# Performance work log

Hardware: AMD Instinct MI355X
Metric: run time of the kernel (lower is better)

The kernel has to match this reference:

```python
import jax, jax.numpy as jnp
import numpy as np

N_AGENT = 32768   # number of agent (dst) nodes
MAX_NBRS = 16     # fixed neighbor count per agent (pad target)
N_NBR = N_AGENT * MAX_NBRS   # nbr (src) nodes
E = N_AGENT * MAX_NBRS       # 1hop edges (grouped by dst)
F_NBR, F_AGENT, F_HOP = 32, 32, 8
H = 128           # critic_hidden_size
N_POW = 4         # n_pow_opts


def _lin(key, fin, fout):
    return jax.random.normal(key, (fin, fout), jnp.float32) / np.sqrt(fin)


def setup_inputs() -> dict:
    key = jax.random.key(0)
    ks = jax.random.split(key, 12)
    return {
        "feat_nbr": jax.random.normal(ks[0], (N_NBR, F_NBR), jnp.float32),
        "feat_agent": jax.random.normal(ks[1], (N_AGENT, F_AGENT), jnp.float32),
        "edge_feat": jax.random.normal(ks[2], (E, F_HOP), jnp.float32),
        "h": jnp.zeros((N_AGENT, H), jnp.float32),
        # NodeGNBlock '1hop': message MLP + update MLP
        "W_msg": _lin(ks[3], F_NBR + F_HOP, H), "b_msg": jnp.zeros((H,), jnp.float32),
        "W_upd": _lin(ks[4], H + F_AGENT, H), "b_upd": jnp.zeros((H,), jnp.float32),
        # RnnLayer: GRUCell(H, H)
        "W_x": _lin(ks[5], H, 3 * H), "W_h": _lin(ks[6], H, 3 * H),
        "b_ih": jnp.zeros((3 * H,), jnp.float32), "b_hh": jnp.zeros((3 * H,), jnp.float32),
        # EdgeGNBlock f_out: edge MLP -> per-edge q over power options, plus agent head
        "W_e1": _lin(ks[7], F_NBR + H + F_HOP, H), "b_e1": jnp.zeros((H,), jnp.float32),
        "W_e2": _lin(ks[8], H, N_POW), "b_e2": jnp.zeros((N_POW,), jnp.float32),
        "W_a": _lin(ks[9], 2 * H, 1), "b_a": jnp.zeros((1,), jnp.float32),
        # graph: each agent has exactly MAX_NBRS incident edges, grouped by dst
        "src_idx": jax.random.randint(ks[10], (E,), 0, N_NBR),
        "dst_idx": jnp.repeat(jnp.arange(N_AGENT), MAX_NBRS),
    }


def reference(feat_nbr, feat_agent, edge_feat, h,
              W_msg, b_msg, W_upd, b_upd,
              W_x, W_h, b_ih, b_hh,
              W_e1, b_e1, W_e2, b_e2, W_a, b_a,
              src_idx, dst_idx):
    act = jax.nn.relu
    # --- NodeGNBlock '1hop': edge message -> sum-aggregate -> node update ---
    m = act(jnp.concatenate([feat_nbr[src_idx], edge_feat], axis=1) @ W_msg + b_msg)  # [E,H]
    agg = jax.ops.segment_sum(m, dst_idx, num_segments=N_AGENT, indices_are_sorted=True)  # [N,H]
    x = act(jnp.concatenate([agg, feat_agent], axis=1) @ W_upd + b_upd)  # [N,H]
    # --- RnnLayer: GRUCell step; output x == new hidden ---
    gi = x @ W_x + b_ih
    gh = h @ W_h + b_hh
    ir, iz, inn = jnp.split(gi, 3, axis=1)
    hr, hz, hn = jnp.split(gh, 3, axis=1)
    r = jax.nn.sigmoid(ir + hr)
    z = jax.nn.sigmoid(iz + hz)
    n = jnp.tanh(inn + r * hn)
    h_new = (1.0 - z) * n + z * h  # [N,H]
    # --- EdgeGNBlock f_out: per-edge q-values + per-agent scalar ---
    ze = act(jnp.concatenate([feat_nbr[src_idx], h_new[dst_idx], edge_feat], axis=1) @ W_e1 + b_e1)  # [E,H]
    nbr_out = ze @ W_e2 + b_e2  # [E, N_POW]
    agg2 = jax.ops.segment_sum(ze, dst_idx, num_segments=N_AGENT, indices_are_sorted=True)
    agent_out = jnp.concatenate([agg2, h_new], axis=1) @ W_a + b_a  # [N,1]
    # --- pad_edge_output: edges grouped by dst with fixed degree -> reshape ---
    padded_nbr_out = nbr_out.reshape(N_AGENT, MAX_NBRS * N_POW)
    q_vals = jnp.concatenate([padded_nbr_out, agent_out], axis=1)  # [N, MAX_NBRS*N_POW+1]
    return q_vals, h_new
```

## Files before the change

### kernel.cpp

```cpp
#include <hip/hip_runtime.h>

typedef _Float16 half_t;
typedef half_t half8 __attribute__((ext_vector_type(8)));
typedef half_t half4 __attribute__((ext_vector_type(4)));
typedef float f32x4 __attribute__((ext_vector_type(4)));
typedef __attribute__((address_space(1))) const void gc_t;
typedef __attribute__((address_space(3))) void ls_t;

#define NAGENT 32768
#define MAXN   16
#define HD     128
#define QCOLS  65
#define QN     (NAGENT * QCOLS)
#define AGB    16
#define EPB    (AGB * MAXN)

#define O_WMT   0
#define O_WE1E  8192
#define O_WE1H  16384
#define O_WUPD  32768
#define O_WX    53248
#define O_WH    102400
#define W_TOTAL 151552

#define MFMA(a, b, c) __builtin_amdgcn_mfma_f32_16x16x32_f16((a), (b), (c), 0, 0, 0)

__global__ void prep_weights(const float* __restrict__ W_msg, const float* __restrict__ W_upd,
                             const float* __restrict__ W_x, const float* __restrict__ W_h,
                             const float* __restrict__ W_e1, half_t* __restrict__ ws) {
    int i = blockIdx.x * 256 + threadIdx.x;
    if (i >= W_TOTAL) return;
    float v; int dst;
    if (i < 8192) {
        int k = i >> 7, n = i & 127;
        v = (k < 40) ? W_msg[k * HD + n] : 0.f;
        dst = O_WMT + n * 64 + k;
    } else if (i < 16384) {
        int j = i - 8192; int k = j >> 7, n = j & 127;
        v = (k < 32) ? W_e1[k * HD + n] : (k < 40 ? W_e1[(160 + k - 32) * HD + n] : 0.f);
        dst = O_WE1E + n * 64 + k;
    } else if (i < 32768) {
        int j = i - 16384; int k = j >> 7, n = j & 127;
        v = W_e1[(32 + k) * HD + n];
        dst = O_WE1H + n * 128 + k;
    } else if (i < 53248) {
        int j = i - 32768; int k = j >> 7, n = j & 127;
        v = W_upd[k * HD + n];
        dst = O_WUPD + n * 160 + k;
    } else if (i < 102400) {
        int j = i - 53248; int k = j / 384, n = j - k * 384;
        v = W_x[k * 384 + n];
        dst = O_WX + n * 128 + k;
    } else {
        int j = i - 102400; int k = j / 384, n = j - k * 384;
        v = W_h[k * 384 + n];
        dst = O_WH + n * 128 + k;
    }
    ws[dst] = (half_t)v;
}

__device__ __forceinline__ half8 ldB(const half_t* __restrict__ WT, int kstride, int n0, int k0, int l) {
    return *(const half8*)(WT + (size_t)(n0 + (l & 15)) * kstride + k0 + ((l >> 4) * 8));
}
__device__ __forceinline__ half4 cvt4(float4 v) {
    return (half4){(half_t)v.x, (half_t)v.y, (half_t)v.z, (half_t)v.w};
}
__device__ __forceinline__ half8 cvt8(float4 a, float4 b) {
    return (half8){(half_t)a.x, (half_t)a.y, (half_t)a.z, (half_t)a.w,
                   (half_t)b.x, (half_t)b.y, (half_t)b.z, (half_t)b.w};
}
__device__ __forceinline__ float sigm(float x) { return 1.f / (1.f + __expf(-x)); }
__device__ __forceinline__ float tanh_fast(float x) { return 1.f - 2.f / (__expf(2.f * x) + 1.f); }

__global__ __launch_bounds__(256, 3) void k_fused(
    const float* __restrict__ feat_nbr, const float* __restrict__ feat_agent,
    const float* __restrict__ edge_feat, const float* __restrict__ h_in,
    const float* __restrict__ b_msg, const float* __restrict__ b_upd,
    const float* __restrict__ b_ih, const float* __restrict__ b_hh,
    const float* __restrict__ b_e1, const float* __restrict__ W_e2,
    const float* __restrict__ b_e2, const float* __restrict__ W_a,
    const float* __restrict__ b_a, const int* __restrict__ src_idx,
    const half_t* __restrict__ ws, float* __restrict__ out)
{
    const int t = threadIdx.x;
    const int w = t >> 6, l = t & 63;
    const int l16 = l & 15, q = l >> 4;
    const int a0 = blockIdx.x * AGB;
    const int be = blockIdx.x * EPB;
    const half8 hz = {0, 0, 0, 0, 0, 0, 0, 0};

    __shared__ float  fng[4][8][64][4];
    __shared__ half_t efh[EPB][8];
    __shared__ half_t bufA[AGB][168];
    __shared__ half_t h_lds[AGB][136];
    __shared__ half_t bufB[AGB][136];
    __shared__ float  hnwa[AGB];

    if (t < AGB) hnwa[t] = 0.f;

    int idx[4];
    #pragma unroll
    for (int mt = 0; mt < 4; ++mt)
        idx[mt] = src_idx[be + w * 64 + mt * 16 + l16];
    #pragma unroll
    for (int mt = 0; mt < 4; ++mt) {
        const float* fr = feat_nbr + (size_t)idx[mt] * 32 + q * 8;
        __builtin_amdgcn_global_load_lds((gc_t*)fr,       (ls_t*)&fng[w][mt * 2][0][0],     16, 0, 0);
        __builtin_amdgcn_global_load_lds((gc_t*)(fr + 4), (ls_t*)&fng[w][mt * 2 + 1][0][0], 16, 0, 0);
    }

    const float* er = edge_feat + (size_t)(be + t) * 8;
    float4 ev0 = *(const float4*)er;
    float4 ev1 = *(const float4*)(er + 4);
    float4 fa_v = {0.f, 0.f, 0.f, 0.f};
    if (t < 128) fa_v = ((const float4*)(feat_agent + (size_t)(a0 + (t >> 3)) * 32))[t & 7];
    float4 h_v0 = ((const float4*)(h_in + (size_t)(a0 + (t >> 5)) * HD))[t & 31];
    float4 h_v1 = ((const float4*)(h_in + (size_t)(a0 + 8 + (t >> 5)) * HD))[t & 31];

    const half_t* wmT = ws + O_WMT;
    half8 Bm[4][4];
    float bm0[4], bm1[4];
    #pragma unroll
    for (int nc = 0; nc < 4; ++nc) {
        const int n0 = nc * 32;
        Bm[nc][0] = ldB(wmT, 64, n0, 0, l);
        Bm[nc][1] = ldB(wmT, 64, n0, 32, l);
        Bm[nc][2] = ldB(wmT, 64, n0 + 16, 0, l);
        Bm[nc][3] = ldB(wmT, 64, n0 + 16, 32, l);
        bm0[nc] = b_msg[n0 + l16];
        bm1[nc] = b_msg[n0 + 16 + l16];
    }

    asm volatile("s_waitcnt vmcnt(0)" ::: "memory");
    __builtin_amdgcn_sched_barrier(0);
    *(half8*)&efh[t][0] = cvt8(ev0, ev1);

    #pragma unroll
    for (int mt = 0; mt < 4; ++mt) {
        const int al = w * 4 + mt;
        const int arow = al * 16 + l16;
        float4 f0 = *(const float4*)&fng[w][mt * 2][l][0];
        float4 f1 = *(const float4*)&fng[w][mt * 2 + 1][l][0];
        half8 af0 = cvt8(f0, f1);
        half8 af1 = (q == 0) ? *(const half8*)&efh[arow][0] : hz;
        #pragma unroll
        for (int nc = 0; nc < 4; ++nc) {
            f32x4 c0 = {0.f, 0.f, 0.f, 0.f}, c1 = {0.f, 0.f, 0.f, 0.f};
            c0 = MFMA(af0, Bm[nc][0], c0);
            c0 = MFMA(af1, Bm[nc][1], c0);
            c1 = MFMA(af0, Bm[nc][2], c1);
            c1 = MFMA(af1, Bm[nc][3], c1);
            float s0 = 0.f, s1 = 0.f;
            #pragma unroll
            for (int r = 0; r < 4; ++r) {
                s0 += fmaxf(c0[r] + bm0[nc], 0.f);
                s1 += fmaxf(c1[r] + bm1[nc], 0.f);
            }
            s0 += __shfl_xor(s0, 16); s0 += __shfl_xor(s0, 32);
            s1 += __shfl_xor(s1, 16); s1 += __shfl_xor(s1, 32);
            if (l < 16) {
                bufA[al][nc * 32 + l]      = (half_t)s0;
                bufA[al][nc * 32 + 16 + l] = (half_t)s1;
            }
        }
    }
    if (t < 128) *(half4*)&bufA[t >> 3][128 + (t & 7) * 4] = cvt4(fa_v);
    *(half4*)&h_lds[t >> 5][(t & 31) * 4] = cvt4(h_v0);
    *(half4*)&h_lds[8 + (t >> 5)][(t & 31) * 4] = cvt4(h_v1);
    __syncthreads();

    {
        const half_t* wupdT = ws + O_WUPD;
        half8 af[5];
        #pragma unroll
        for (int k = 0; k < 5; ++k) af[k] = *(const half8*)&bufA[l16][k * 32 + q * 8];
        #pragma unroll
        for (int s = 0; s < 2; ++s) {
            const int n0 = (w * 2 + s) * 16;
            f32x4 c = {0.f, 0.f, 0.f, 0.f};
            #pragma unroll
            for (int k = 0; k < 5; ++k) c = MFMA(af[k], ldB(wupdT, 160, n0, k * 32, l), c);
            float bu = b_upd[n0 + l16];
            #pragma unroll
            for (int r = 0; r < 4; ++r)
                bufB[q * 4 + r][n0 + l16] = (half_t)fmaxf(c[r] + bu, 0.f);
        }
    }
    __syncthreads();

    {
        const half_t* wxT = ws + O_WX;
        const half_t* whT = ws + O_WH;
        half8 ax[4], ah[4];
        #pragma unroll
        for (int k = 0; k < 4; ++k) {
            ax[k] = *(const half8*)&bufB[l16][k * 32 + q * 8];
            ah[k] = *(const half8*)&h_lds[l16][k * 32 + q * 8];
        }
        float pa[4] = {0.f, 0.f, 0.f, 0.f};
        #pragma unroll
        for (int s = 0; s < 2; ++s) {
            const int colb = w * 32 + s * 16;
            f32x4 gi[3], gh[3];
            #pragma unroll
            for (int g = 0; g < 3; ++g) {
                const int n0 = g * 128 + colb;
                f32x4 ci = {0.f, 0.f, 0.f, 0.f}, ch = {0.f, 0.f, 0.f, 0.f};
                #pragma unroll
                for (int k = 0; k < 4; ++k) {
                    ci = MFMA(ax[k], ldB(wxT, 128, n0, k * 32, l), ci);
                    ch = MFMA(ah[k], ldB(whT, 128, n0, k * 32, l), ch);
                }
                gi[g] = ci; gh[g] = ch;
            }
            const int col = colb + l16;
            float bi0 = b_ih[col], bi1 = b_ih[HD + col], bi2 = b_ih[2 * HD + col];
            float bh0 = b_hh[col], bh1 = b_hh[HD + col], bh2 = b_hh[2 * HD + col];
            float wac = W_a[HD + col];
            #pragma unroll
            for (int r = 0; r < 4; ++r) {
                const int row = q * 4 + r;
                float rg = sigm(gi[0][r] + bi0 + gh[0][r] + bh0);
                float zg = sigm(gi[1][r] + bi1 + gh[1][r] + bh1);
                float ng = tanh_fast(gi[2][r] + bi2 + rg * (gh[2][r] + bh2));
                float hv = (1.f - zg) * ng + zg * (float)h_lds[row][col];
                out[QN + (size_t)(a0 + row) * HD + col] = hv;
                bufA[row][col] = (half_t)hv;
                pa[r] = fmaf(hv, wac, pa[r]);
            }
        }
        #pragma unroll
        for (int r = 0; r < 4; ++r) {
            #pragma unroll
            for (int m = 1; m <= 8; m <<= 1) pa[r] += __shfl_xor(pa[r], m);
            if (l16 == 0) atomicAdd(&hnwa[q * 4 + r], pa[r]);
        }
    }
    __syncthreads();

    {
        const half_t* we1hT = ws + O_WE1H;
        half8 an[4];
        #pragma unroll
        for (int k = 0; k < 4; ++k) an[k] = *(const half8*)&bufA[l16][k * 32 + q * 8];
        #pragma unroll
        for (int s = 0; s < 2; ++s) {
            const int n0 = (w * 2 + s) * 16;
            f32x4 c = {0.f, 0.f, 0.f, 0.f};
            #pragma unroll
            for (int k = 0; k < 4; ++k) c = MFMA(an[k], ldB(we1hT, 128, n0, k * 32, l), c);
            float bv = b_e1[n0 + l16];
            #pragma unroll
            for (int r = 0; r < 4; ++r)
                bufB[q * 4 + r][n0 + l16] = (half_t)(c[r] + bv);
        }
    }
    __syncthreads();

    {
        const half_t* we1eT = ws + O_WE1E;
        half8 B[4][4];
        float wa0[4], wa1[4];
        #pragma unroll
        for (int nc = 0; nc < 4; ++nc) {
            const int n0 = nc * 32;
            B[nc][0] = ldB(we1eT, 64, n0, 0, l);
            B[nc][1] = ldB(we1eT, 64, n0, 32, l);
            B[nc][2] = ldB(we1eT, 64, n0 + 16, 0, l);
            B[nc][3] = ldB(we1eT, 64, n0 + 16, 32, l);
            wa0[nc] = W_a[n0 + l16];
            wa1[nc] = W_a[n0 + 16 + l16];
        }
        const float ba = b_a[0];

        #pragma unroll
        for (int mt = 0; mt < 4; ++mt) {
            const int al = w * 4 + mt;
            const int arow = al * 16 + l16;
            float4 f0 = *(const float4*)&fng[w][mt * 2][l][0];
            float4 f1 = *(const float4*)&fng[w][mt * 2 + 1][l][0];
            half8 af0 = cvt8(f0, f1);
            half8 af1 = hz;
            if (q == 0) af1 = *(const half8*)&efh[arow][0];
            float qa[4][4];
            #pragma unroll
            for (int r = 0; r < 4; ++r)
                #pragma unroll
                for (int p = 0; p < 4; ++p) qa[r][p] = 0.f;
            float wa_part = 0.f;
            #pragma unroll
            for (int nc = 0; nc < 4; ++nc) {
                const int n0 = nc * 32;
                f32x4 c0 = {0.f, 0.f, 0.f, 0.f}, c1 = {0.f, 0.f, 0.f, 0.f};
                c0 = MFMA(af0, B[nc][0], c0);
                c0 = MFMA(af1, B[nc][1], c0);
                c1 = MFMA(af0, B[nc][2], c1);
                c1 = MFMA(af1, B[nc][3], c1);
                const int col0 = n0 + l16, col1 = n0 + 16 + l16;
                float ch0 = (float)bufB[al][col0], ch1 = (float)bufB[al][col1];
                float4 w20 = *(const float4*)(W_e2 + col0 * 4);
                float4 w21 = *(const float4*)(W_e2 + col1 * 4);
                float s0 = 0.f, s1 = 0.f;
                #pragma unroll
                for (int r = 0; r < 4; ++r) {
                    float z0 = fmaxf(c0[r] + ch0, 0.f);
                    float z1 = fmaxf(c1[r] + ch1, 0.f);
                    s0 += z0; s1 += z1;
                    qa[r][0] = fmaf(z0, w20.x, fmaf(z1, w21.x, qa[r][0]));
                    qa[r][1] = fmaf(z0, w20.y, fmaf(z1, w21.y, qa[r][1]));
                    qa[r][2] = fmaf(z0, w20.z, fmaf(z1, w21.z, qa[r][2]));
                    qa[r][3] = fmaf(z0, w20.w, fmaf(z1, w21.w, qa[r][3]));
                }
                s0 += __shfl_xor(s0, 16); s0 += __shfl_xor(s0, 32);
                s1 += __shfl_xor(s1, 16); s1 += __shfl_xor(s1, 32);
                wa_part = fmaf(s0, wa0[nc], fmaf(s1, wa1[nc], wa_part));
            }
            #pragma unroll
            for (int m = 1; m <= 8; m <<= 1)
                #pragma unroll
                for (int r = 0; r < 4; ++r)
                    #pragma unroll
                    for (int p = 0; p < 4; ++p) qa[r][p] += __shfl_xor(qa[r][p], m);
            if (l16 < 4) {
                const int p = l16;
                const float bz = b_e2[p];
                #pragma unroll
                for (int r = 0; r < 4; ++r)
                    out[(size_t)(a0 + al) * QCOLS + (q * 4 + r) * 4 + p] = qa[r][p] + bz;
            }
            #pragma unroll
            for (int m = 1; m <= 8; m <<= 1) wa_part += __shfl_xor(wa_part, m);
            if (l == 0)
                out[(size_t)(a0 + al) * QCOLS + 64] = wa_part + hnwa[al] + ba;
        }
    }
}

extern "C" void kernel_launch(void* const* d_in, const int* in_sizes, int n_in,
                              void* d_out, int out_size, void* d_ws, size_t ws_size,
                              hipStream_t stream) {
    const float* feat_nbr   = (const float*)d_in[0];
    const float* feat_agent = (const float*)d_in[1];
    const float* edge_feat  = (const float*)d_in[2];
    const float* h_in       = (const float*)d_in[3];
    const float* W_msg = (const float*)d_in[4];
    const float* b_msg = (const float*)d_in[5];
    const float* W_upd = (const float*)d_in[6];
    const float* b_upd = (const float*)d_in[7];
    const float* W_x   = (const float*)d_in[8];
    const float* W_h   = (const float*)d_in[9];
    const float* b_ih  = (const float*)d_in[10];
    const float* b_hh  = (const float*)d_in[11];
    const float* W_e1  = (const float*)d_in[12];
    const float* b_e1  = (const float*)d_in[13];
    const float* W_e2  = (const float*)d_in[14];
    const float* b_e2  = (const float*)d_in[15];
    const float* W_a   = (const float*)d_in[16];
    const float* b_a   = (const float*)d_in[17];
    const int* src_idx = (const int*)d_in[18];
    half_t* ws = (half_t*)d_ws;
    float* out = (float*)d_out;
    const int nblk = NAGENT / AGB;

    prep_weights<<<(W_TOTAL + 255) / 256, 256, 0, stream>>>(W_msg, W_upd, W_x, W_h, W_e1, ws);
    k_fused<<<nblk, 256, 0, stream>>>(feat_nbr, feat_agent, edge_feat, h_in,
                                      b_msg, b_upd, b_ih, b_hh, b_e1,
                                      W_e2, b_e2, W_a, b_a, src_idx, ws, out);
}
```

Measured before the change: 325.7 us.

## Pre-convert neighbor and edge features to fp16 and gather half-precision rows

Adds a prep kernel that converts feat_nbr and edge_feat to fp16 in the workspace, and a new fused kernel that gathers these half rows straight into LDS with global_load_lds. The goal is to halve the bytes moved by the random gather and drop the per-block float-to-half conversion. The weight prep now writes its output coalesced, and the new kernel asks for occupancy 4. The cost is an extra full pass over the feature arrays (read fp32, write fp16) every call, and the path is used only when the workspace is large enough.

New measurement: 368.1 us. +13.0%, slower.

```diff
diff --git a/kernel.cpp b/kernel.cpp
--- a/kernel.cpp
+++ b/kernel.cpp
@@ -14,6 +14,8 @@
 #define QN     (NAGENT * QCOLS)
 #define AGB    16
 #define EPB    (AGB * MAXN)
+#define NNBR   (NAGENT * MAXN)
+#define NEDGE  (NAGENT * MAXN)
 
 #define O_WMT   0
 #define O_WE1E  8192
@@ -22,57 +24,328 @@
 #define O_WX    53248
 #define O_WH    102400
 #define W_TOTAL 151552
+#define O_FN16  151552
+#define O_EF16  (O_FN16 + NNBR * 32)
+#define WS_F16_NEED ((size_t)(O_EF16 + (size_t)NEDGE * 8) * 2)
 
 #define MFMA(a, b, c) __builtin_amdgcn_mfma_f32_16x16x32_f16((a), (b), (c), 0, 0, 0)
+
+__device__ __forceinline__ half4 cvt4(float4 v) {
+    return (half4){(half_t)v.x, (half_t)v.y, (half_t)v.z, (half_t)v.w};
+}
+__device__ __forceinline__ half8 cvt8(float4 a, float4 b) {
+    return (half8){(half_t)a.x, (half_t)a.y, (half_t)a.z, (half_t)a.w,
+                   (half_t)b.x, (half_t)b.y, (half_t)b.z, (half_t)b.w};
+}
 
 __global__ void prep_weights(const float* __restrict__ W_msg, const float* __restrict__ W_upd,
                              const float* __restrict__ W_x, const float* __restrict__ W_h,
                              const float* __restrict__ W_e1, half_t* __restrict__ ws) {
     int i = blockIdx.x * 256 + threadIdx.x;
     if (i >= W_TOTAL) return;
-    float v; int dst;
+    float v;
     if (i < 8192) {
-        int k = i >> 7, n = i & 127;
+        int n = i >> 6, k = i & 63;
         v = (k < 40) ? W_msg[k * HD + n] : 0.f;
-        dst = O_WMT + n * 64 + k;
     } else if (i < 16384) {
-        int j = i - 8192; int k = j >> 7, n = j & 127;
+        int j = i - 8192; int n = j >> 6, k = j & 63;
         v = (k < 32) ? W_e1[k * HD + n] : (k < 40 ? W_e1[(160 + k - 32) * HD + n] : 0.f);
-        dst = O_WE1E + n * 64 + k;
     } else if (i < 32768) {
-        int j = i - 16384; int k = j >> 7, n = j & 127;
+        int j = i - 16384; int n = j >> 7, k = j & 127;
         v = W_e1[(32 + k) * HD + n];
-        dst = O_WE1H + n * 128 + k;
     } else if (i < 53248) {
-        int j = i - 32768; int k = j >> 7, n = j & 127;
+        int j = i - 32768; int n = j / 160, k = j - n * 160;
         v = W_upd[k * HD + n];
-        dst = O_WUPD + n * 160 + k;
     } else if (i < 102400) {
-        int j = i - 53248; int k = j / 384, n = j - k * 384;
+        int j = i - 53248; int n = j >> 7, k = j & 127;
         v = W_x[k * 384 + n];
-        dst = O_WX + n * 128 + k;
     } else {
-        int j = i - 102400; int k = j / 384, n = j - k * 384;
+        int j = i - 102400; int n = j >> 7, k = j & 127;
         v = W_h[k * 384 + n];
-        dst = O_WH + n * 128 + k;
-    }
-    ws[dst] = (half_t)v;
+    }
+    ws[i] = (half_t)v;
+}
+
+__global__ void prep_feats(const float* __restrict__ fn, const float* __restrict__ ef,
+                           half_t* __restrict__ ws) {
+    half_t* fnh = ws + O_FN16;
+    half_t* efh = ws + O_EF16;
+    const int NU_FN = NNBR * 32 / 8;
+    const int NU_EF = NEDGE * 8 / 8;
+    for (int u = blockIdx.x * 256 + threadIdx.x; u < NU_FN + NU_EF; u += gridDim.x * 256) {
+        const float* s; half_t* d;
+        if (u < NU_FN) { s = fn + (size_t)u * 8; d = fnh + (size_t)u * 8; }
+        else { int z = u - NU_FN; s = ef + (size_t)z * 8; d = efh + (size_t)z * 8; }
+        float4 a = *(const float4*)s, b = *(const float4*)(s + 4);
+        *(half8*)d = cvt8(a, b);
+    }
 }
 
 __device__ __forceinline__ half8 ldB(const half_t* __restrict__ WT, int kstride, int n0, int k0, int l) {
     return *(const half8*)(WT + (size_t)(n0 + (l & 15)) * kstride + k0 + ((l >> 4) * 8));
 }
-__device__ __forceinline__ half4 cvt4(float4 v) {
-    return (half4){(half_t)v.x, (half_t)v.y, (half_t)v.z, (half_t)v.w};
-}
-__device__ __forceinline__ half8 cvt8(float4 a, float4 b) {
-    return (half8){(half_t)a.x, (half_t)a.y, (half_t)a.z, (half_t)a.w,
-                   (half_t)b.x, (half_t)b.y, (half_t)b.z, (half_t)b.w};
-}
 __device__ __forceinline__ float sigm(float x) { return 1.f / (1.f + __expf(-x)); }
 __device__ __forceinline__ float tanh_fast(float x) { return 1.f - 2.f / (__expf(2.f * x) + 1.f); }
 
-__global__ __launch_bounds__(256, 3) void k_fused(
+__global__ __launch_bounds__(256, 4) void k_fused_h(
+    const float* __restrict__ feat_agent, const float* __restrict__ h_in,
+    const float* __restrict__ b_msg, const float* __restrict__ b_upd,
+    const float* __restrict__ b_ih, const float* __restrict__ b_hh,
+    const float* __restrict__ b_e1, const float* __restrict__ W_e2,
+    const float* __restrict__ b_e2, const float* __restrict__ W_a,
+    const float* __restrict__ b_a, const int* __restrict__ src_idx,
+    const half_t* __restrict__ ws, float* __restrict__ out)
+{
+    const int t = threadIdx.x;
+    const int w = t >> 6, l = t & 63;
+    const int l16 = l & 15, q = l >> 4;
+    const int a0 = blockIdx.x * AGB;
+    const int be = blockIdx.x * EPB;
+    const half8 hz = {0, 0, 0, 0, 0, 0, 0, 0};
+
+    __shared__ half_t fng16[4][4][512];
+    __shared__ half_t efh[EPB][8];
+    __shared__ half_t bufA[AGB][168];
+    __shared__ half_t h_lds[AGB][136];
+    __shared__ half_t bufB[AGB][136];
+    __shared__ float  hnwa[AGB];
+
+    if (t < AGB) hnwa[t] = 0.f;
+
+    int idx[4];
+    #pragma unroll
+    for (int mt = 0; mt < 4; ++mt)
+        idx[mt] = src_idx[be + w * 64 + mt * 16 + l16];
+    const half_t* fnh = ws + O_FN16;
+    const half_t* efg = ws + O_EF16;
+    #pragma unroll
+    for (int mt = 0; mt < 4; ++mt) {
+        const half_t* fr = fnh + (size_t)idx[mt] * 32 + q * 8;
+        __builtin_amdgcn_global_load_lds((gc_t*)fr, (ls_t*)&fng16[w][mt][0], 16, 0, 0);
+    }
+    __builtin_amdgcn_global_load_lds((gc_t*)(efg + (size_t)(be + w * 64 + l) * 8),
+                                     (ls_t*)&efh[w * 64][0], 16, 0, 0);
+
+    float4 fa_v = {0.f, 0.f, 0.f, 0.f};
+    if (t < 128) fa_v = ((const float4*)(feat_agent + (size_t)(a0 + (t >> 3)) * 32))[t & 7];
+    float4 h_v0 = ((const float4*)(h_in + (size_t)(a0 + (t >> 5)) * HD))[t & 31];
+    float4 h_v1 = ((const float4*)(h_in + (size_t)(a0 + 8 + (t >> 5)) * HD))[t & 31];
+
+    const half_t* wmT = ws + O_WMT;
+    half8 Bm[4][4];
+    float bm0[4], bm1[4];
+    #pragma unroll
+    for (int nc = 0; nc < 4; ++nc) {
+        const int n0 = nc * 32;
+        Bm[nc][0] = ldB(wmT, 64, n0, 0, l);
+        Bm[nc][1] = ldB(wmT, 64, n0, 32, l);
+        Bm[nc][2] = ldB(wmT, 64, n0 + 16, 0, l);
+        Bm[nc][3] = ldB(wmT, 64, n0 + 16, 32, l);
+        bm0[nc] = b_msg[n0 + l16];
+        bm1[nc] = b_msg[n0 + 16 + l16];
+    }
+
+    asm volatile("s_waitcnt vmcnt(0)" ::: "memory");
+    __builtin_amdgcn_sched_barrier(0);
+
+    #pragma unroll
+    for (int mt = 0; mt < 4; ++mt) {
+        const int al = w * 4 + mt;
+        const int arow = al * 16 + l16;
+        half8 af0 = *(const half8*)&fng16[w][mt][l * 8];
+        half8 af1 = (q == 0) ? *(const half8*)&efh[arow][0] : hz;
+        #pragma unroll
+        for (int nc = 0; nc < 4; ++nc) {
+            f32x4 c0 = {0.f, 0.f, 0.f, 0.f}, c1 = {0.f, 0.f, 0.f, 0.f};
+            c0 = MFMA(af0, Bm[nc][0], c0);
+            c0 = MFMA(af1, Bm[nc][1], c0);
+            c1 = MFMA(af0, Bm[nc][2], c1);
+            c1 = MFMA(af1, Bm[nc][3], c1);
+            float s0 = 0.f, s1 = 0.f;
+            #pragma unroll
+            for (int r = 0; r < 4; ++r) {
+                s0 += fmaxf(c0[r] + bm0[nc], 0.f);
+                s1 += fmaxf(c1[r] + bm1[nc], 0.f);
+            }
+            s0 += __shfl_xor(s0, 16); s0 += __shfl_xor(s0, 32);
+            s1 += __shfl_xor(s1, 16); s1 += __shfl_xor(s1, 32);
+            if (l < 16) {
+                bufA[al][nc * 32 + l]      = (half_t)s0;
+                bufA[al][nc * 32 + 16 + l] = (half_t)s1;
+            }
+        }
+    }
+    if (t < 128) *(half4*)&bufA[t >> 3][128 + (t & 7) * 4] = cvt4(fa_v);
+    *(half4*)&h_lds[t >> 5][(t & 31) * 4] = cvt4(h_v0);
+    *(half4*)&h_lds[8 + (t >> 5)][(t & 31) * 4] = cvt4(h_v1);
+    __syncthreads();
+
+    {
+        const half_t* wupdT = ws + O_WUPD;
+        half8 af[5];
+        #pragma unroll
+        for (int k = 0; k < 5; ++k) af[k] = *(const half8*)&bufA[l16][k * 32 + q * 8];
+        #pragma unroll
+        for (int s = 0; s < 2; ++s) {
+            const int n0 = (w * 2 + s) * 16;
+            f32x4 c = {0.f, 0.f, 0.f, 0.f};
+            #pragma unroll
+            for (int k = 0; k < 5; ++k) c = MFMA(af[k], ldB(wupdT, 160, n0, k * 32, l), c);
+            float bu = b_upd[n0 + l16];
+            #pragma unroll
+            for (int r = 0; r < 4; ++r)
+                bufB[q * 4 + r][n0 + l16] = (half_t)fmaxf(c[r] + bu, 0.f);
+        }
+    }
+    __syncthreads();
+
+    {
+        const half_t* wxT = ws + O_WX;
+        const half_t* whT = ws + O_WH;
+        half8 ax[4], ah[4];
+        #pragma unroll
+        for (int k = 0; k < 4; ++k) {
+            ax[k] = *(const half8*)&bufB[l16][k * 32 + q * 8];
+            ah[k] = *(const half8*)&h_lds[l16][k * 32 + q * 8];
+        }
+        float pa[4] = {0.f, 0.f, 0.f, 0.f};
+        #pragma unroll
+        for (int s = 0; s < 2; ++s) {
+            const int colb = w * 32 + s * 16;
+            f32x4 gi[3], gh[3];
+            #pragma unroll
+            for (int g = 0; g < 3; ++g) {
+                const int n0 = g * 128 + colb;
+                f32x4 ci = {0.f, 0.f, 0.f, 0.f}, ch = {0.f, 0.f, 0.f, 0.f};
+                #pragma unroll
+                for (int k = 0; k < 4; ++k) {
+                    ci = MFMA(ax[k], ldB(wxT, 128, n0, k * 32, l), ci);
+                    ch = MFMA(ah[k], ldB(whT, 128, n0, k * 32, l), ch);
+                }
+                gi[g] = ci; gh[g] = ch;
+            }
+            const int col = colb + l16;
+            float bi0 = b_ih[col], bi1 = b_ih[HD + col], bi2 = b_ih[2 * HD + col];
+            float bh0 = b_hh[col], bh1 = b_hh[HD + col], bh2 = b_hh[2 * HD + col];
+            float wac = W_a[HD + col];
+            #pragma unroll
+            for (int r = 0; r < 4; ++r) {
+                const int row = q * 4 + r;
+                float rg = sigm(gi[0][r] + bi0 + gh[0][r] + bh0);
+                float zg = sigm(gi[1][r] + bi1 + gh[1][r] + bh1);
+                float ng = tanh_fast(gi[2][r] + bi2 + rg * (gh[2][r] + bh2));
+                float hv = (1.f - zg) * ng + zg * (float)h_lds[row][col];
+                out[QN + (size_t)(a0 + row) * HD + col] = hv;
+                bufA[row][col] = (half_t)hv;
+                pa[r] = fmaf(hv, wac, pa[r]);
+            }
+        }
+        #pragma unroll
+        for (int r = 0; r < 4; ++r) {
+            #pragma unroll
+            for (int m = 1; m <= 8; m <<= 1) pa[r] += __shfl_xor(pa[r], m);
+            if (l16 == 0) atomicAdd(&hnwa[q * 4 + r], pa[r]);
+        }
+    }
+    __syncthreads();
+
+    {
+        const half_t* we1hT = ws + O_WE1H;
+        half8 an[4];
+        #pragma unroll
+        for (int k = 0; k < 4; ++k) an[k] = *(const half8*)&bufA[l16][k * 32 + q * 8];
+        #pragma unroll
+        for (int s = 0; s < 2; ++s) {
+            const int n0 = (w * 2 + s) * 16;
+            f32x4 c = {0.f, 0.f, 0.f, 0.f};
+            #pragma unroll
+            for (int k = 0; k < 4; ++k) c = MFMA(an[k], ldB(we1hT, 128, n0, k * 32, l), c);
+            float bv = b_e1[n0 + l16];
+            #pragma unroll
+            for (int r = 0; r < 4; ++r)
+                bufB[q * 4 + r][n0 + l16] = (half_t)(c[r] + bv);
+        }
+    }
+    __syncthreads();
+
+    {
+        const half_t* we1eT = ws + O_WE1E;
+        half8 B[4][4];
+        float wa0[4], wa1[4];
+        #pragma unroll
+        for (int nc = 0; nc < 4; ++nc) {
+            const int n0 = nc * 32;
+            B[nc][0] = ldB(we1eT, 64, n0, 0, l);
+            B[nc][1] = ldB(we1eT, 64, n0, 32, l);
+            B[nc][2] = ldB(we1eT, 64, n0 + 16, 0, l);
+            B[nc][3] = ldB(we1eT, 64, n0 + 16, 32, l);
+            wa0[nc] = W_a[n0 + l16];
+            wa1[nc] = W_a[n0 + 16 + l16];
+        }
+        const float ba = b_a[0];
+
+        #pragma unroll
+        for (int mt = 0; mt < 4; ++mt) {
+            const int al = w * 4 + mt;
+            const int arow = al * 16 + l16;
+            half8 af0 = *(const half8*)&fng16[w][mt][l * 8];
+            half8 af1 = hz;
+            if (q == 0) af1 = *(const half8*)&efh[arow][0];
+            float qa[4][4];
+            #pragma unroll
+            for (int r = 0; r < 4; ++r)
+                #pragma unroll
+                for (int p = 0; p < 4; ++p) qa[r][p] = 0.f;
+            float wa_part = 0.f;
+            #pragma unroll
+            for (int nc = 0; nc < 4; ++nc) {
+                const int n0 = nc * 32;
+                f32x4 c0 = {0.f, 0.f, 0.f, 0.f}, c1 = {0.f, 0.f, 0.f, 0.f};
+                c0 = MFMA(af0, B[nc][0], c0);
+                c0 = MFMA(af1, B[nc][1], c0);
+                c1 = MFMA(af0, B[nc][2], c1);
+                c1 = MFMA(af1, B[nc][3], c1);
+                const int col0 = n0 + l16, col1 = n0 + 16 + l16;
+                float ch0 = (float)bufB[al][col0], ch1 = (float)bufB[al][col1];
+                float4 w20 = *(const float4*)(W_e2 + col0 * 4);
+                float4 w21 = *(const float4*)(W_e2 + col1 * 4);
+                float s0 = 0.f, s1 = 0.f;
+                #pragma unroll
+                for (int r = 0; r < 4; ++r) {
+                    float z0 = fmaxf(c0[r] + ch0, 0.f);
+                    float z1 = fmaxf(c1[r] + ch1, 0.f);
+                    s0 += z0; s1 += z1;
+                    qa[r][0] = fmaf(z0, w20.x, fmaf(z1, w21.x, qa[r][0]));
+                    qa[r][1] = fmaf(z0, w20.y, fmaf(z1, w21.y, qa[r][1]));
+                    qa[r][2] = fmaf(z0, w20.z, fmaf(z1, w21.z, qa[r][2]));
+                    qa[r][3] = fmaf(z0, w20.w, fmaf(z1, w21.w, qa[r][3]));
+                }
+                s0 += __shfl_xor(s0, 16); s0 += __shfl_xor(s0, 32);
+                s1 += __shfl_xor(s1, 16); s1 += __shfl_xor(s1, 32);
+                wa_part = fmaf(s0, wa0[nc], fmaf(s1, wa1[nc], wa_part));
+            }
+            #pragma unroll
+            for (int m = 1; m <= 8; m <<= 1)
+                #pragma unroll
+                for (int r = 0; r < 4; ++r)
+                    #pragma unroll
+                    for (int p = 0; p < 4; ++p) qa[r][p] += __shfl_xor(qa[r][p], m);
+            if (l16 < 4) {
+                const int p = l16;
+                const float bz = b_e2[p];
+                #pragma unroll
+                for (int r = 0; r < 4; ++r)
+                    out[(size_t)(a0 + al) * QCOLS + (q * 4 + r) * 4 + p] = qa[r][p] + bz;
+            }
+            #pragma unroll
+            for (int m = 1; m <= 8; m <<= 1) wa_part += __shfl_xor(wa_part, m);
+            if (l == 0)
+                out[(size_t)(a0 + al) * QCOLS + 64] = wa_part + hnwa[al] + ba;
+        }
+    }
+}
+
+__global__ __launch_bounds__(256, 3) void k_fused_f32(
     const float* __restrict__ feat_nbr, const float* __restrict__ feat_agent,
     const float* __restrict__ edge_feat, const float* __restrict__ h_in,
     const float* __restrict__ b_msg, const float* __restrict__ b_upd,
@@ -363,7 +636,14 @@
     const int nblk = NAGENT / AGB;
 
     prep_weights<<<(W_TOTAL + 255) / 256, 256, 0, stream>>>(W_msg, W_upd, W_x, W_h, W_e1, ws);
-    k_fused<<<nblk, 256, 0, stream>>>(feat_nbr, feat_agent, edge_feat, h_in,
-                                      b_msg, b_upd, b_ih, b_hh, b_e1,
-                                      W_e2, b_e2, W_a, b_a, src_idx, ws, out);
-}
+    if (ws_size >= WS_F16_NEED) {
+        prep_feats<<<2048, 256, 0, stream>>>(feat_nbr, edge_feat, ws);
+        k_fused_h<<<nblk, 256, 0, stream>>>(feat_agent, h_in,
+                                            b_msg, b_upd, b_ih, b_hh, b_e1,
+                                            W_e2, b_e2, W_a, b_a, src_idx, ws, out);
+    } else {
+        k_fused_f32<<<nblk, 256, 0, stream>>>(feat_nbr, feat_agent, edge_feat, h_in,
+                                              b_msg, b_upd, b_ih, b_hh, b_e1,
+                                              W_e2, b_e2, W_a, b_a, src_idx, ws, out);
+    }
+}
```

## Halve gather staging LDS, keep neighbor fragments in registers, raise occupancy target

Applied to the files above, without the earlier changes.

The neighbor-feature gather buffer is cut in half and filled in two rounds: the first two tiles are loaded, converted to fp16 register fragments, and then the buffer is refilled with the remaining tiles while the first tiles' message MFMAs run. The converted fragments are kept in registers and reused by the final edge stage instead of being re-read from LDS. The freed region is reused for the hidden-state and intermediate tiles, and launch bounds move from 3 to 4 blocks per CU to take advantage of the smaller LDS footprint. Weight prep now writes coalesced by output index. The risk is extra register pressure from the held fragments under the tighter register budget, which could cause spills.

After: 349.4 us. 1.07x slower.

```diff
diff --git a/kernel.cpp b/kernel.cpp
--- a/kernel.cpp
+++ b/kernel.cpp
@@ -30,33 +30,27 @@
                              const float* __restrict__ W_e1, half_t* __restrict__ ws) {
     int i = blockIdx.x * 256 + threadIdx.x;
     if (i >= W_TOTAL) return;
-    float v; int dst;
+    float v;
     if (i < 8192) {
-        int k = i >> 7, n = i & 127;
+        int n = i >> 6, k = i & 63;
         v = (k < 40) ? W_msg[k * HD + n] : 0.f;
-        dst = O_WMT + n * 64 + k;
     } else if (i < 16384) {
-        int j = i - 8192; int k = j >> 7, n = j & 127;
+        int j = i - 8192; int n = j >> 6, k = j & 63;
         v = (k < 32) ? W_e1[k * HD + n] : (k < 40 ? W_e1[(160 + k - 32) * HD + n] : 0.f);
-        dst = O_WE1E + n * 64 + k;
     } else if (i < 32768) {
-        int j = i - 16384; int k = j >> 7, n = j & 127;
+        int j = i - 16384; int n = j >> 7, k = j & 127;
         v = W_e1[(32 + k) * HD + n];
-        dst = O_WE1H + n * 128 + k;
     } else if (i < 53248) {
-        int j = i - 32768; int k = j >> 7, n = j & 127;
+        int j = i - 32768; int n = j / 160, k = j - n * 160;
         v = W_upd[k * HD + n];
-        dst = O_WUPD + n * 160 + k;
     } else if (i < 102400) {
-        int j = i - 53248; int k = j / 384, n = j - k * 384;
+        int j = i - 53248; int n = j >> 7, k = j & 127;
         v = W_x[k * 384 + n];
-        dst = O_WX + n * 128 + k;
     } else {
-        int j = i - 102400; int k = j / 384, n = j - k * 384;
+        int j = i - 102400; int n = j >> 7, k = j & 127;
         v = W_h[k * 384 + n];
-        dst = O_WH + n * 128 + k;
-    }
-    ws[dst] = (half_t)v;
+    }
+    ws[i] = (half_t)v;
 }
 
 __device__ __forceinline__ half8 ldB(const half_t* __restrict__ WT, int kstride, int n0, int k0, int l) {
@@ -72,7 +66,7 @@
 __device__ __forceinline__ float sigm(float x) { return 1.f / (1.f + __expf(-x)); }
 __device__ __forceinline__ float tanh_fast(float x) { return 1.f - 2.f / (__expf(2.f * x) + 1.f); }
 
-__global__ __launch_bounds__(256, 3) void k_fused(
+__global__ __launch_bounds__(256, 4) void k_fused(
     const float* __restrict__ feat_nbr, const float* __restrict__ feat_agent,
     const float* __restrict__ edge_feat, const float* __restrict__ h_in,
     const float* __restrict__ b_msg, const float* __restrict__ b_upd,
@@ -89,12 +83,12 @@
     const int be = blockIdx.x * EPB;
     const half8 hz = {0, 0, 0, 0, 0, 0, 0, 0};
 
-    __shared__ float  fng[4][8][64][4];
+    __shared__ __align__(16) char raw[16384];
     __shared__ half_t efh[EPB][8];
     __shared__ half_t bufA[AGB][168];
-    __shared__ half_t h_lds[AGB][136];
-    __shared__ half_t bufB[AGB][136];
     __shared__ float  hnwa[AGB];
+
+    float* fngw = (float*)raw + (w << 10);
 
     if (t < AGB) hnwa[t] = 0.f;
 
@@ -103,10 +97,10 @@
     for (int mt = 0; mt < 4; ++mt)
         idx[mt] = src_idx[be + w * 64 + mt * 16 + l16];
     #pragma unroll
-    for (int mt = 0; mt < 4; ++mt) {
+    for (int mt = 0; mt < 2; ++mt) {
         const float* fr = feat_nbr + (size_t)idx[mt] * 32 + q * 8;
-        __builtin_amdgcn_global_load_lds((gc_t*)fr,       (ls_t*)&fng[w][mt * 2][0][0],     16, 0, 0);
-        __builtin_amdgcn_global_load_lds((gc_t*)(fr + 4), (ls_t*)&fng[w][mt * 2 + 1][0][0], 16, 0, 0);
+        __builtin_amdgcn_global_load_lds((gc_t*)fr,       (ls_t*)(fngw + (mt * 2) * 256),     16, 0, 0);
+        __builtin_amdgcn_global_load_lds((gc_t*)(fr + 4), (ls_t*)(fngw + (mt * 2 + 1) * 256), 16, 0, 0);
     }
 
     const float* er = edge_feat + (size_t)(be + t) * 8;
@@ -134,14 +128,29 @@
     asm volatile("s_waitcnt vmcnt(0)" ::: "memory");
     __builtin_amdgcn_sched_barrier(0);
     *(half8*)&efh[t][0] = cvt8(ev0, ev1);
-
+    if (t < 128) *(half4*)&bufA[t >> 3][128 + (t & 7) * 4] = cvt4(fa_v);
+
+    half8 af0k[4];
+    {
+        float4 a0v = *(const float4*)(fngw + 0 * 256 + l * 4);
+        float4 a1v = *(const float4*)(fngw + 1 * 256 + l * 4);
+        float4 b0v = *(const float4*)(fngw + 2 * 256 + l * 4);
+        float4 b1v = *(const float4*)(fngw + 3 * 256 + l * 4);
+        af0k[0] = cvt8(a0v, a1v);
+        af0k[1] = cvt8(b0v, b1v);
+    }
+    asm volatile("s_waitcnt lgkmcnt(0)" ::: "memory");
+    __builtin_amdgcn_sched_barrier(0);
     #pragma unroll
-    for (int mt = 0; mt < 4; ++mt) {
+    for (int mt = 2; mt < 4; ++mt) {
+        const float* fr = feat_nbr + (size_t)idx[mt] * 32 + q * 8;
+        __builtin_amdgcn_global_load_lds((gc_t*)fr,       (ls_t*)(fngw + ((mt - 2) * 2) * 256),     16, 0, 0);
+        __builtin_amdgcn_global_load_lds((gc_t*)(fr + 4), (ls_t*)(fngw + ((mt - 2) * 2 + 1) * 256), 16, 0, 0);
+    }
+
+    auto phA = [&](int mt, half8 af0) {
         const int al = w * 4 + mt;
         const int arow = al * 16 + l16;
-        float4 f0 = *(const float4*)&fng[w][mt * 2][l][0];
-        float4 f1 = *(const float4*)&fng[w][mt * 2 + 1][l][0];
-        half8 af0 = cvt8(f0, f1);
         half8 af1 = (q == 0) ? *(const half8*)&efh[arow][0] : hz;
         #pragma unroll
         for (int nc = 0; nc < 4; ++nc) {
@@ -163,11 +172,29 @@
                 bufA[al][nc * 32 + 16 + l] = (half_t)s1;
             }
         }
-    }
-    if (t < 128) *(half4*)&bufA[t >> 3][128 + (t & 7) * 4] = cvt4(fa_v);
-    *(half4*)&h_lds[t >> 5][(t & 31) * 4] = cvt4(h_v0);
-    *(half4*)&h_lds[8 + (t >> 5)][(t & 31) * 4] = cvt4(h_v1);
+    };
+    phA(0, af0k[0]);
+    phA(1, af0k[1]);
+
+    asm volatile("s_waitcnt vmcnt(0)" ::: "memory");
+    __builtin_amdgcn_sched_barrier(0);
+    {
+        float4 a0v = *(const float4*)(fngw + 0 * 256 + l * 4);
+        float4 a1v = *(const float4*)(fngw + 1 * 256 + l * 4);
+        float4 b0v = *(const float4*)(fngw + 2 * 256 + l * 4);
+        float4 b1v = *(const float4*)(fngw + 3 * 256 + l * 4);
+        af0k[2] = cvt8(a0v, a1v);
+        af0k[3] = cvt8(b0v, b1v);
+    }
+    phA(2, af0k[2]);
+    phA(3, af0k[3]);
+
     __syncthreads();
+
+    half_t* hl = (half_t*)raw;
+    half_t* xb = (half_t*)raw + 2176;
+    *(half4*)&hl[(t >> 5) * 136 + (t & 31) * 4] = cvt4(h_v0);
+    *(half4*)&hl[(8 + (t >> 5)) * 136 + (t & 31) * 4] = cvt4(h_v1);
 
     {
         const half_t* wupdT = ws + O_WUPD;
@@ -183,7 +210,7 @@
             float bu = b_upd[n0 + l16];
             #pragma unroll
             for (int r = 0; r < 4; ++r)
-                bufB[q * 4 + r][n0 + l16] = (half_t)fmaxf(c[r] + bu, 0.f);
+                xb[(q * 4 + r) * 136 + n0 + l16] = (half_t)fmaxf(c[r] + bu, 0.f);
         }
     }
     __syncthreads();
@@ -194,8 +221,8 @@
         half8 ax[4], ah[4];
         #pragma unroll
         for (int k = 0; k < 4; ++k) {
-            ax[k] = *(const half8*)&bufB[l16][k * 32 + q * 8];
-            ah[k] = *(const half8*)&h_lds[l16][k * 32 + q * 8];
+            ax[k] = *(const half8*)&xb[l16 * 136 + k * 32 + q * 8];
+            ah[k] = *(const half8*)&hl[l16 * 136 + k * 32 + q * 8];
         }
         float pa[4] = {0.f, 0.f, 0.f, 0.f};
         #pragma unroll
@@ -223,7 +250,7 @@
                 float rg = sigm(gi[0][r] + bi0 + gh[0][r] + bh0);
                 float zg = sigm(gi[1][r] + bi1 + gh[1][r] + bh1);
                 float ng = tanh_fast(gi[2][r] + bi2 + rg * (gh[2][r] + bh2));
-                float hv = (1.f - zg) * ng + zg * (float)h_lds[row][col];
+                float hv = (1.f - zg) * ng + zg * (float)hl[row * 136 + col];
                 out[QN + (size_t)(a0 + row) * HD + col] = hv;
                 bufA[row][col] = (half_t)hv;
                 pa[r] = fmaf(hv, wac, pa[r]);
@@ -252,7 +279,7 @@
             float bv = b_e1[n0 + l16];
             #pragma unroll
             for (int r = 0; r < 4; ++r)
-                bufB[q * 4 + r][n0 + l16] = (half_t)(c[r] + bv);
+                xb[(q * 4 + r) * 136 + n0 + l16] = (half_t)(c[r] + bv);
         }
     }
     __syncthreads();
@@ -273,13 +300,9 @@
         }
         const float ba = b_a[0];
 
-        #pragma unroll
-        for (int mt = 0; mt < 4; ++mt) {
+        auto phC = [&](int mt, half8 af0) {
             const int al = w * 4 + mt;
             const int arow = al * 16 + l16;
-            float4 f0 = *(const float4*)&fng[w][mt * 2][l][0];
-            float4 f1 = *(const float4*)&fng[w][mt * 2 + 1][l][0];
-            half8 af0 = cvt8(f0, f1);
             half8 af1 = hz;
             if (q == 0) af1 = *(const half8*)&efh[arow][0];
             float qa[4][4];
@@ -297,7 +320,7 @@
                 c1 = MFMA(af0, B[nc][2], c1);
                 c1 = MFMA(af1, B[nc][3], c1);
                 const int col0 = n0 + l16, col1 = n0 + 16 + l16;
-                float ch0 = (float)bufB[al][col0], ch1 = (float)bufB[al][col1];
+                float ch0 = (float)xb[al * 136 + col0], ch1 = (float)xb[al * 136 + col1];
                 float4 w20 = *(const float4*)(W_e2 + col0 * 4);
                 float4 w21 = *(const float4*)(W_e2 + col1 * 4);
                 float s0 = 0.f, s1 = 0.f;
@@ -332,7 +355,11 @@
             for (int m = 1; m <= 8; m <<= 1) wa_part += __shfl_xor(wa_part, m);
             if (l == 0)
                 out[(size_t)(a0 + al) * QCOLS + 64] = wa_part + hnwa[al] + ba;
-        }
+        };
+        phC(0, af0k[0]);
+        phC(1, af0k[1]);
+        phC(2, af0k[2]);
+        phC(3, af0k[3]);
     }
 }
 
```
